# Performance work log

Hardware: AMD Instinct MI355X
Metric: run time of the kernel (lower is better)

## Reference

```python
import jax, jax.numpy as jnp
import numpy as np
from jax import lax

N_GAUSS = 8192
SEM_DIM = 32


def setup_inputs() -> dict:
    key = jax.random.key(0)
    k1, k2, k3, k4, k5 = jax.random.split(key, 5)
    H, W = 1024, 1024
    # centers sampled inside the view frustum of an identity-pose pinhole camera
    z = jax.random.uniform(k1, (N_GAUSS,), minval=0.5, maxval=6.0)
    xy = jax.random.uniform(k2, (N_GAUSS, 2), minval=-0.6, maxval=0.6) * z[:, None]
    centers = jnp.concatenate([xy, z[:, None]], axis=1).astype(jnp.float32)
    colors = jax.random.uniform(k3, (N_GAUSS, 3), dtype=jnp.float32)
    opacities = jax.random.uniform(k4, (N_GAUSS, 1), dtype=jnp.float32)
    sem_feats = jax.random.normal(k5, (N_GAUSS, SEM_DIM), dtype=jnp.float32) * 0.1
    camera_pose = jnp.eye(4, dtype=jnp.float32)
    fx = fy = 800.0
    camera_intrinsics = jnp.array([[fx, 0.0, W / 2.0], [0.0, fy, H / 2.0], [0.0, 0.0, 1.0]], dtype=jnp.float32)
    return {
        "centers": centers,
        "colors": colors,
        "opacities": opacities,
        "sem_feats": sem_feats,
        "camera_pose": camera_pose,
        "camera_intrinsics": camera_intrinsics,
        "H": H,
        "W": W,
    }


def reference(centers, colors, opacities, sem_feats, camera_pose, camera_intrinsics, H, W):
    # Differentiable point-splat alpha compositing (faithful to render_gaussians).
    # Torch recurrence per pixel: alpha_i = o_i * (1 - A), A += alpha_i
    # => transmittance before i equals prod_{j<i, same pixel, nearer depth}(1 - o_j).
    N = centers.shape[0]
    cam = centers @ camera_pose[:3, :3].T + camera_pose[:3, 3]  # (N,3)
    z = cam[:, 2]
    valid = z > 0.1
    proj = cam @ camera_intrinsics.T  # (N,3)
    denom = jnp.where(valid, proj[:, 2], 1.0)
    # .long() in torch truncates toward zero; astype(int32) matches for the kept range
    px = (proj[:, 0] / denom).astype(jnp.int32)
    py = (proj[:, 1] / denom).astype(jnp.int32)
    ok = valid & (px >= 0) & (px < W) & (py >= 0) & (py < H)
    pid = jnp.where(ok, py * W + px, H * W)  # invalid -> dump bucket
    o = jnp.where(ok, opacities[:, 0], 0.0)
    depth = jnp.where(ok, z, jnp.inf)
    # sort primarily by pixel, secondarily by depth (front-to-back within pixel)
    order = jnp.lexsort((depth, pid))
    pid_s = pid[order]
    o_s = o[order]
    feats = jnp.concatenate([colors, sem_feats], axis=1)[order]  # (N, 3+D)
    # segmented exclusive cumprod of (1 - o) in log space
    log_t = jnp.log1p(-jnp.clip(o_s, 0.0, 1.0 - 1e-7))
    csum = jnp.cumsum(log_t)
    excl = csum - log_t
    boundary = jnp.concatenate([jnp.array([True]), pid_s[1:] != pid_s[:-1]])
    start_idx = lax.cummax(jnp.where(boundary, jnp.arange(N), 0))
    T = jnp.exp(excl - excl[start_idx])  # transmittance before each splat
    alpha = o_s * T
    out_flat = jax.ops.segment_sum(alpha[:, None] * feats, pid_s, num_segments=H * W + 1)[: H * W]
    feat_dim = feats.shape[1]
    return out_flat.T.reshape(feat_dim, H, W)
```

## Files before the change

### kernel.cpp

```cpp
#include <hip/hip_runtime.h>
#include <stdint.h>


__global__ __launch_bounds__(256) void gs_project_kernel(
        const float* __restrict__ centers, const float* __restrict__ opac,
        const float* __restrict__ pose, const float* __restrict__ Km,
        const int* __restrict__ Hp, const int* __restrict__ Wp,
        unsigned int* __restrict__ pid_a, unsigned int* __restrict__ dep_a,
        float* __restrict__ opa_a, unsigned int* __restrict__ table, int N) {
    int i = blockIdx.x * blockDim.x + threadIdx.x;
    if (i >= N) return;
    const int H = *Hp, W = *Wp;
    float x = centers[3 * i], y = centers[3 * i + 1], zc = centers[3 * i + 2];
    float cxx = pose[0] * x + pose[1] * y + pose[2]  * zc + pose[3];
    float cyy = pose[4] * x + pose[5] * y + pose[6]  * zc + pose[7];
    float czz = pose[8] * x + pose[9] * y + pose[10] * zc + pose[11];
    bool valid = czz > 0.1f;
    float p0 = Km[0] * cxx + Km[1] * cyy + Km[2] * czz;
    float p1 = Km[3] * cxx + Km[4] * cyy + Km[5] * czz;
    float p2 = Km[6] * cxx + Km[7] * cyy + Km[8] * czz;
    float denom = valid ? p2 : 1.0f;
    int px = (int)(p0 / denom);
    int py = (int)(p1 / denom);
    bool ok = valid && px >= 0 && px < W && py >= 0 && py < H;
    unsigned int pid = ok ? (unsigned int)(py * W + px) : (unsigned int)(H * W);
    pid_a[i] = pid;
    dep_a[i] = __float_as_uint(czz);
    opa_a[i] = ok ? opac[i] : 0.0f;
    if (ok) atomicAdd(&table[pid], 1u);
}

__global__ __launch_bounds__(256) void gs_splat_kernel(
        const unsigned int* __restrict__ pid_a, const unsigned int* __restrict__ dep_a,
        const float* __restrict__ opa_a,
        const unsigned int* __restrict__ table,
        const float* __restrict__ colors, const float* __restrict__ sem,
        float* __restrict__ out, int N, int sem_dim, int HW) {
    const int t = threadIdx.x;
    const int lane = t & 63;
    const int wave = t >> 6;
    const int i = blockIdx.x * 4 + wave;
    if (i >= N) return;

    const unsigned int pid_i = pid_a[i];
    if (pid_i >= (unsigned int)HW) return;
    const float oi = opa_a[i];

    const unsigned int cnt = table[pid_i];
    const bool unique = (cnt == 1u);
    float prod = 1.0f;
    if (!unique) {
        const unsigned int di = dep_a[i];
        const uint4* p4 = (const uint4*)pid_a;
        const int nq = N >> 2;
        for (int q = lane; q < nq; q += 64) {
            uint4 p = p4[q];
            int j0 = q << 2;
            #pragma unroll
            for (int k = 0; k < 4; ++k) {
                unsigned int pj = (k == 0) ? p.x : (k == 1) ? p.y : (k == 2) ? p.z : p.w;
                int j = j0 + k;
                if (pj == pid_i && j != i) {
                    unsigned int dj = dep_a[j];
                    if (dj < di || (dj == di && j < i)) {
                        prod *= 1.0f - fminf(fmaxf(opa_a[j], 0.0f), 1.0f - 1e-7f);
                    }
                }
            }
        }
        for (int off = 32; off > 0; off >>= 1) prod *= __shfl_xor(prod, off, 64);
    }

    const float alpha = oi * prod;
    const int fd = 3 + sem_dim;
    if (lane < fd) {
        float f = (lane < 3) ? colors[3 * i + lane] : sem[sem_dim * i + (lane - 3)];
        float* dst = &out[(size_t)lane * (size_t)HW + pid_i];
        float v = alpha * f;
        if (unique) *dst = v;
        else        atomicAdd(dst, v);
    }
}

extern "C" void kernel_launch(void* const* d_in, const int* in_sizes, int n_in,
                              void* d_out, int out_size, void* d_ws, size_t ws_size,
                              hipStream_t stream) {
    const float* centers = (const float*)d_in[0];
    const float* colors  = (const float*)d_in[1];
    const float* opac    = (const float*)d_in[2];
    const float* sem     = (const float*)d_in[3];
    const float* pose    = (const float*)d_in[4];
    const float* Km      = (const float*)d_in[5];
    const int*   Hp      = (const int*)d_in[6];
    const int*   Wp      = (const int*)d_in[7];

    int N = in_sizes[0] / 3;
    int sem_dim = in_sizes[3] / N;
    int fd = 3 + sem_dim;
    int HW = out_size / fd;

    char* ws = (char*)d_ws;
    unsigned int* pid_a  = (unsigned int*)(ws);
    unsigned int* dep_a  = (unsigned int*)(ws + 32 * 1024);
    float*        opa_a  = (float*)      (ws + 64 * 1024);
    unsigned int* table  = (unsigned int*)(ws + 128 * 1024);

    hipMemsetAsync(d_out, 0, (size_t)out_size * sizeof(float), stream);
    hipMemsetAsync(table, 0, (size_t)HW * sizeof(unsigned int), stream);

    gs_project_kernel<<<(N + 255) / 256, 256, 0, stream>>>(
        centers, opac, pose, Km, Hp, Wp, pid_a, dep_a, opa_a, table, N);

    gs_splat_kernel<<<(N + 3) / 4, 256, 0, stream>>>(
        pid_a, dep_a, opa_a, table, colors, sem,
        (float*)d_out, N, sem_dim, HW);
}
```

Before: 180.2 us.

## Pack count and splat index into pixel table and gather-write output

```diff
diff --git a/kernel.cpp b/kernel.cpp
--- a/kernel.cpp
+++ b/kernel.cpp
@@ -27,13 +27,66 @@
     pid_a[i] = pid;
     dep_a[i] = __float_as_uint(czz);
     opa_a[i] = ok ? opac[i] : 0.0f;
-    if (ok) atomicAdd(&table[pid], 1u);
+    if (ok) atomicAdd(&table[pid], (1u << 24) | (unsigned int)i);
 }
 
-__global__ __launch_bounds__(256) void gs_splat_kernel(
+__global__ __launch_bounds__(256) void gs_gather_kernel(
+        const unsigned int* __restrict__ table,
+        const float* __restrict__ opa_a,
+        const float* __restrict__ colors, const float* __restrict__ sem,
+        float* __restrict__ out, int HW, int sem_dim) {
+    const int q = blockIdx.x * blockDim.x + threadIdx.x;
+    const int nq = HW >> 2;
+    if (q >= nq) return;
+    const int fd = 3 + sem_dim;
+    uint4 rec4 = ((const uint4*)table)[q];
+    float4* dst = (float4*)out + q;
+
+    if ((rec4.x | rec4.y | rec4.z | rec4.w) == 0u) {
+        const float4 z = make_float4(0.f, 0.f, 0.f, 0.f);
+        for (int pl = 0; pl < fd; ++pl) dst[(size_t)pl * nq] = z;
+    } else {
+        unsigned int r[4] = {rec4.x, rec4.y, rec4.z, rec4.w};
+        int   idx[4];
+        float a[4];
+        #pragma unroll
+        for (int k = 0; k < 4; ++k) {
+            idx[k] = (int)(r[k] & 0xFFFFFFu);
+            a[k] = ((r[k] >> 24) == 1u) ? opa_a[idx[k]] : 0.0f;
+        }
+        for (int pl = 0; pl < fd; ++pl) {
+            float v[4];
+            #pragma unroll
+            for (int k = 0; k < 4; ++k) {
+                float f = 0.0f;
+                if (a[k] != 0.0f)
+                    f = (pl < 3) ? colors[3 * idx[k] + pl]
+                                 : sem[sem_dim * idx[k] + (pl - 3)];
+                v[k] = a[k] * f;
+            }
+            dst[(size_t)pl * nq] = make_float4(v[0], v[1], v[2], v[3]);
+        }
+    }
+
+    if (q == 0) {
+        for (int pix = nq << 2; pix < HW; ++pix) {
+            unsigned int r = table[pix];
+            int   id = (int)(r & 0xFFFFFFu);
+            float a  = ((r >> 24) == 1u) ? opa_a[id] : 0.0f;
+            for (int pl = 0; pl < fd; ++pl) {
+                float f = 0.0f;
+                if (a != 0.0f)
+                    f = (pl < 3) ? colors[3 * id + pl]
+                                 : sem[sem_dim * id + (pl - 3)];
+                out[(size_t)pl * HW + pix] = a * f;
+            }
+        }
+    }
+}
+
+__global__ __launch_bounds__(256) void gs_collide_kernel(
         const unsigned int* __restrict__ pid_a, const unsigned int* __restrict__ dep_a,
-        const float* __restrict__ opa_a,
-        const unsigned int* __restrict__ table,
+        const float* __restrict__ opa_a, const unsigned int* __restrict__ table,
         const float* __restrict__ colors, const float* __restrict__ sem,
         float* __restrict__ out, int N, int sem_dim, int HW) {
     const int t = threadIdx.x;
@@ -44,41 +97,35 @@
 
     const unsigned int pid_i = pid_a[i];
     if (pid_i >= (unsigned int)HW) return;
+    if ((table[pid_i] >> 24) <= 1u) return;
+
     const float oi = opa_a[i];
-
-    const unsigned int cnt = table[pid_i];
-    const bool unique = (cnt == 1u);
+    const unsigned int di = dep_a[i];
     float prod = 1.0f;
-    if (!unique) {
-        const unsigned int di = dep_a[i];
-        const uint4* p4 = (const uint4*)pid_a;
-        const int nq = N >> 2;
-        for (int q = lane; q < nq; q += 64) {
-            uint4 p = p4[q];
-            int j0 = q << 2;
-            #pragma unroll
-            for (int k = 0; k < 4; ++k) {
-                unsigned int pj = (k == 0) ? p.x : (k == 1) ? p.y : (k == 2) ? p.z : p.w;
-                int j = j0 + k;
-                if (pj == pid_i && j != i) {
-                    unsigned int dj = dep_a[j];
-                    if (dj < di || (dj == di && j < i)) {
-                        prod *= 1.0f - fminf(fmaxf(opa_a[j], 0.0f), 1.0f - 1e-7f);
-                    }
+    const uint4* p4 = (const uint4*)pid_a;
+    const int nq = N >> 2;
+    for (int q = lane; q < nq; q += 64) {
+        uint4 p = p4[q];
+        int j0 = q << 2;
+        #pragma unroll
+        for (int k = 0; k < 4; ++k) {
+            unsigned int pj = (k == 0) ? p.x : (k == 1) ? p.y : (k == 2) ? p.z : p.w;
+            int j = j0 + k;
+            if (pj == pid_i && j != i) {
+                unsigned int dj = dep_a[j];
+                if (dj < di || (dj == di && j < i)) {
+                    prod *= 1.0f - fminf(fmaxf(opa_a[j], 0.0f), 1.0f - 1e-7f);
                 }
             }
         }
-        for (int off = 32; off > 0; off >>= 1) prod *= __shfl_xor(prod, off, 64);
     }
+    for (int off = 32; off > 0; off >>= 1) prod *= __shfl_xor(prod, off, 64);
 
     const float alpha = oi * prod;
     const int fd = 3 + sem_dim;
     if (lane < fd) {
         float f = (lane < 3) ? colors[3 * i + lane] : sem[sem_dim * i + (lane - 3)];
-        float* dst = &out[(size_t)lane * (size_t)HW + pid_i];
-        float v = alpha * f;
-        if (unique) *dst = v;
-        else        atomicAdd(dst, v);
+        atomicAdd(&out[(size_t)lane * (size_t)HW + pid_i], alpha * f);
     }
 }
 
@@ -105,13 +152,16 @@
     float*        opa_a  = (float*)      (ws + 64 * 1024);
     unsigned int* table  = (unsigned int*)(ws + 128 * 1024);
 
-    hipMemsetAsync(d_out, 0, (size_t)out_size * sizeof(float), stream);
     hipMemsetAsync(table, 0, (size_t)HW * sizeof(unsigned int), stream);
 
     gs_project_kernel<<<(N + 255) / 256, 256, 0, stream>>>(
         centers, opac, pose, Km, Hp, Wp, pid_a, dep_a, opa_a, table, N);
 
-    gs_splat_kernel<<<(N + 3) / 4, 256, 0, stream>>>(
+    int nq = HW >> 2;
+    gs_gather_kernel<<<(nq + 255) / 256, 256, 0, stream>>>(
+        table, opa_a, colors, sem, (float*)d_out, HW, sem_dim);
+
+    gs_collide_kernel<<<(N + 3) / 4, 256, 0, stream>>>(
         pid_a, dep_a, opa_a, table, colors, sem,
         (float*)d_out, N, sem_dim, HW);
 }
```

Measured after the change: 197.3 us. 9.5% more time.
